# Performance work log

Hardware: AMD Instinct MI355X
Metric: run time of the kernel (lower is better)

The kernel has to match this reference:

```python
import jax, jax.numpy as jnp
import numpy as np

NUM_NODES = 100000
NUM_REL_P1 = 238  # num_relations + 1 (extra column for self-connection relation id -1)
B = 32768
S = 16
D_IN = 256
D_OUT = 256


def setup_inputs() -> dict:
    key = jax.random.key(0)
    k1, k2, k3, k4, k5 = jax.random.split(key, 5)
    neighbors = jax.random.randint(k1, (B, S), 0, NUM_NODES)          # sampled neighbor node ids
    relations = jax.random.randint(k2, (B, S), 0, NUM_REL_P1)          # sampled relation ids
    features = jax.random.normal(k3, (NUM_NODES, D_IN), dtype=jnp.float32)
    weight = jax.random.normal(k4, (D_OUT, D_IN), dtype=jnp.float32) * (1.0 / np.sqrt(D_IN))
    relation_weight = jax.random.normal(k5, (D_OUT, NUM_REL_P1), dtype=jnp.float32) * 0.05
    return {"neighbors": neighbors, "relations": relations, "features": features,
            "weight": weight, "relation_weight": relation_weight}


def reference(neighbors, relations, features, weight, relation_weight):
    # gather sampled neighbor embeddings: [B, S, D_in]
    neighbor_emb = features[neighbors]
    # mean-aggregate over the sample dim: [B, D_in]
    agg_neighbors = neighbor_emb.mean(axis=1)
    # linear transform: [B, D_in] @ [D_in, D_out] -> [B, D_out]
    agg_neighbors = agg_neighbors @ weight.T
    # gather + mean relation embeddings: [B, S, D_out] -> [B, D_out]
    agg_relations = relation_weight.T[relations].mean(axis=1)
    return jax.nn.relu(agg_neighbors + agg_relations)
```

## Files before the change

kernel.cpp:

```cpp
#include <hip/hip_runtime.h>

#define B_ROWS  32768
#define S_SAMP  16
#define NRELS   238
#define DIM     256
#define N_NODES 100000
#define NF4     ((N_NODES * DIM) / 4)
#define CONV_BLOCKS (NF4 / 256)

typedef __attribute__((ext_vector_type(8))) short  short8;
typedef __attribute__((ext_vector_type(8))) unsigned short ushort8;
typedef __attribute__((ext_vector_type(4))) float  f32x4;

static __device__ __forceinline__ unsigned short f2bf(float f) {
    unsigned int u = __float_as_uint(f);
    u += 0x7FFFu + ((u >> 16) & 1u);
    return (unsigned short)(u >> 16);
}
static __device__ __forceinline__ float bf2f(unsigned short u) {
    return __uint_as_float(((unsigned int)u) << 16);
}

__global__ __launch_bounds__(256) void prep_kernel(const float* __restrict__ F,
                                                   const float* __restrict__ W,
                                                   const float* __restrict__ RW,
                                                   unsigned short* __restrict__ Fb,
                                                   unsigned short* __restrict__ Wb,
                                                   unsigned short* __restrict__ RWb) {
    if (blockIdx.x < CONV_BLOCKS) {
        int i = blockIdx.x * 256 + threadIdx.x;
        float4 v = ((const float4*)F)[i];
        ushort4 p;
        p.x = f2bf(v.x); p.y = f2bf(v.y); p.z = f2bf(v.z); p.w = f2bf(v.w);
        ((ushort4*)Fb)[i] = p;
    } else {
        int i = (blockIdx.x - CONV_BLOCKS) * 256 + threadIdx.x;
        if (i < DIM * DIM) {
            Wb[i] = f2bf(W[i]);
            int n = i >> 8;
            int k = i & 255;
            RWb[i] = (k < NRELS) ? f2bf(RW[n * NRELS + k]) : (unsigned short)0;
        }
    }
}

__global__ __launch_bounds__(512, 8) void fused_kernel(const int* __restrict__ nbr,
                                                       const int* __restrict__ rels,
                                                       const unsigned short* __restrict__ Fb,
                                                       const unsigned short* __restrict__ RWb,
                                                       const unsigned short* __restrict__ Wb,
                                                       float* __restrict__ out) {
    __shared__ unsigned short As[32][264];
    __shared__ unsigned short Cs[32][264];
    __shared__ unsigned int   cnt4[32][32];
    const int tid  = threadIdx.x;
    const int lane = tid & 63;
    const int wid  = __builtin_amdgcn_readfirstlane(tid >> 6);
    const int half = lane >> 5;
    const int li   = lane & 31;
    const int col0 = lane & 15;
    const int quad = lane >> 4;
    const int r0g  = blockIdx.x * 32;

    unsigned int* c4 = (unsigned int*)cnt4;
    c4[tid] = 0u; c4[tid + 512] = 0u;
    __syncthreads();

    {
        int rid = rels[r0g * S_SAMP + tid];
        atomicAdd(&cnt4[tid >> 4][rid >> 3], 1u << ((rid & 7) * 4));
    }

    const float sc = 1.0f / 16.0f;
    for (int i = 0; i < 4; ++i) {
        const int row_l = wid * 4 + i;
        const int row_g = r0g + row_l;
        const int2* nb2 = (const int2*)(nbr + row_g * S_SAMP);
        float af[8] = {0.f, 0.f, 0.f, 0.f, 0.f, 0.f, 0.f, 0.f};
#pragma unroll
        for (int t = 0; t < 8; ++t) {
            int2 nn = nb2[t];
            int nid = half ? nn.y : nn.x;
            ushort8 f = *(const ushort8*)(Fb + (size_t)nid * DIM + li * 8);
#pragma unroll
            for (int j = 0; j < 8; ++j) af[j] += bf2f(f[j]);
        }
        ushort8 pk;
#pragma unroll
        for (int j = 0; j < 8; ++j) {
            float full = af[j] + __shfl_xor(af[j], 32, 64);
            pk[j] = f2bf(full * sc);
        }
        if (!half) *(ushort8*)&As[row_l][li * 8] = pk;
    }
    __syncthreads();

    {
        const int rr = tid >> 4;
        const int w2 = tid & 15;
#pragma unroll
        for (int g = 0; g < 2; ++g) {
            unsigned int w = cnt4[rr][w2 * 2 + g];
            ushort8 ck;
#pragma unroll
            for (int j = 0; j < 8; ++j)
                ck[j] = f2bf((float)((w >> (4 * j)) & 0xFu) * 0.0625f);
            *(ushort8*)&Cs[rr][(w2 * 2 + g) * 8] = ck;
        }
    }
    __syncthreads();

    f32x4 acc[2][2];
#pragma unroll
    for (int mt = 0; mt < 2; ++mt)
#pragma unroll
        for (int j = 0; j < 2; ++j) acc[mt][j] = (f32x4){0.f, 0.f, 0.f, 0.f};

#pragma unroll
    for (int s = 0; s < 2; ++s) {
        const unsigned short* Bp = s ? RWb : Wb;
#pragma unroll
        for (int kh = 0; kh < 4; ++kh) {
            short8 Breg[2][2];
#pragma unroll
            for (int j = 0; j < 2; ++j)
#pragma unroll
                for (int kk = 0; kk < 2; ++kk)
                    Breg[j][kk] = *(const short8*)(Bp + (size_t)((wid * 2 + j) * 16 + col0) * DIM
                                                      + (kh * 2 + kk) * 32 + quad * 8);
#pragma unroll
            for (int mt = 0; mt < 2; ++mt) {
                const int mrow = mt * 16 + col0;
#pragma unroll
                for (int kk = 0; kk < 2; ++kk) {
                    short8 a;
                    if (s == 0) a = *(const short8*)&As[mrow][(kh * 2 + kk) * 32 + quad * 8];
                    else        a = *(const short8*)&Cs[mrow][(kh * 2 + kk) * 32 + quad * 8];
#pragma unroll
                    for (int j = 0; j < 2; ++j)
                        acc[mt][j] = __builtin_amdgcn_mfma_f32_16x16x32_bf16(a, Breg[j][kk], acc[mt][j], 0, 0, 0);
                }
            }
        }
    }

#pragma unroll
    for (int mt = 0; mt < 2; ++mt) {
#pragma unroll
        for (int j = 0; j < 2; ++j) {
            const int col = (wid * 2 + j) * 16 + col0;
#pragma unroll
            for (int i2 = 0; i2 < 4; ++i2) {
                const int r_l = mt * 16 + quad * 4 + i2;
                float v = acc[mt][j][i2];
                out[(size_t)(r0g + r_l) * DIM + col] = v > 0.f ? v : 0.f;
            }
        }
    }
}

extern "C" void kernel_launch(void* const* d_in, const int* in_sizes, int n_in,
                              void* d_out, int out_size, void* d_ws, size_t ws_size,
                              hipStream_t stream) {
    const int*   neighbors = (const int*)d_in[0];
    const int*   relations = (const int*)d_in[1];
    const float* features  = (const float*)d_in[2];
    const float* weight    = (const float*)d_in[3];
    const float* relw      = (const float*)d_in[4];
    float* out = (float*)d_out;

    char* ws = (char*)d_ws;
    unsigned short* Wb  = (unsigned short*)ws;
    unsigned short* RWb = (unsigned short*)(ws + 131072);
    unsigned short* Fb  = (unsigned short*)(ws + 262144);

    prep_kernel<<<CONV_BLOCKS + 256, 256, 0, stream>>>(features, weight, relw, Fb, Wb, RWb);
    fused_kernel<<<B_ROWS / 32, 512, 0, stream>>>(neighbors, relations, Fb, RWb, Wb, out);
}
```

Before: 224.3 us.

## Shrink fused kernel tile to 16 rows with 256-thread blocks

```diff
diff --git a/kernel.cpp b/kernel.cpp
--- a/kernel.cpp
+++ b/kernel.cpp
@@ -44,15 +44,15 @@
     }
 }
 
-__global__ __launch_bounds__(512, 8) void fused_kernel(const int* __restrict__ nbr,
+__global__ __launch_bounds__(256, 8) void fused_kernel(const int* __restrict__ nbr,
                                                        const int* __restrict__ rels,
                                                        const unsigned short* __restrict__ Fb,
                                                        const unsigned short* __restrict__ RWb,
                                                        const unsigned short* __restrict__ Wb,
                                                        float* __restrict__ out) {
-    __shared__ unsigned short As[32][264];
-    __shared__ unsigned short Cs[32][264];
-    __shared__ unsigned int   cnt4[32][32];
+    __shared__ unsigned short As[16][264];
+    __shared__ unsigned short Cs[16][264];
+    __shared__ unsigned int   cnt4[16][32];
     const int tid  = threadIdx.x;
     const int lane = tid & 63;
     const int wid  = __builtin_amdgcn_readfirstlane(tid >> 6);
@@ -60,10 +60,10 @@
     const int li   = lane & 31;
     const int col0 = lane & 15;
     const int quad = lane >> 4;
-    const int r0g  = blockIdx.x * 32;
+    const int r0g  = blockIdx.x * 16;
 
     unsigned int* c4 = (unsigned int*)cnt4;
-    c4[tid] = 0u; c4[tid + 512] = 0u;
+    c4[tid] = 0u; c4[tid + 256] = 0u;
     __syncthreads();
 
     {
@@ -97,64 +97,48 @@
 
     {
         const int rr = tid >> 4;
-        const int w2 = tid & 15;
+        const int w2 = (tid & 15) * 2;
 #pragma unroll
         for (int g = 0; g < 2; ++g) {
-            unsigned int w = cnt4[rr][w2 * 2 + g];
+            unsigned int w = cnt4[rr][w2 + g];
             ushort8 ck;
 #pragma unroll
             for (int j = 0; j < 8; ++j)
                 ck[j] = f2bf((float)((w >> (4 * j)) & 0xFu) * 0.0625f);
-            *(ushort8*)&Cs[rr][(w2 * 2 + g) * 8] = ck;
+            *(ushort8*)&Cs[rr][(w2 + g) * 8] = ck;
         }
     }
     __syncthreads();
 
-    f32x4 acc[2][2];
+    f32x4 acc[4];
 #pragma unroll
-    for (int mt = 0; mt < 2; ++mt)
+    for (int j = 0; j < 4; ++j) acc[j] = (f32x4){0.f, 0.f, 0.f, 0.f};
+
+#pragma unroll 2
+    for (int ks = 0; ks < 16; ++ks) {
+        const unsigned short* Bp = (ks < 8) ? Wb : RWb;
+        const int kk = ks & 7;
+        short8 Breg[4];
 #pragma unroll
-        for (int j = 0; j < 2; ++j) acc[mt][j] = (f32x4){0.f, 0.f, 0.f, 0.f};
-
+        for (int j = 0; j < 4; ++j)
+            Breg[j] = *(const short8*)(Bp + (size_t)(wid * 64 + j * 16 + col0) * DIM
+                                          + kk * 32 + quad * 8);
+        short8 a;
+        if (ks < 8) a = *(const short8*)&As[col0][kk * 32 + quad * 8];
+        else        a = *(const short8*)&Cs[col0][kk * 32 + quad * 8];
 #pragma unroll
-    for (int s = 0; s < 2; ++s) {
-        const unsigned short* Bp = s ? RWb : Wb;
-#pragma unroll
-        for (int kh = 0; kh < 4; ++kh) {
-            short8 Breg[2][2];
-#pragma unroll
-            for (int j = 0; j < 2; ++j)
-#pragma unroll
-                for (int kk = 0; kk < 2; ++kk)
-                    Breg[j][kk] = *(const short8*)(Bp + (size_t)((wid * 2 + j) * 16 + col0) * DIM
-                                                      + (kh * 2 + kk) * 32 + quad * 8);
-#pragma unroll
-            for (int mt = 0; mt < 2; ++mt) {
-                const int mrow = mt * 16 + col0;
-#pragma unroll
-                for (int kk = 0; kk < 2; ++kk) {
-                    short8 a;
-                    if (s == 0) a = *(const short8*)&As[mrow][(kh * 2 + kk) * 32 + quad * 8];
-                    else        a = *(const short8*)&Cs[mrow][(kh * 2 + kk) * 32 + quad * 8];
-#pragma unroll
-                    for (int j = 0; j < 2; ++j)
-                        acc[mt][j] = __builtin_amdgcn_mfma_f32_16x16x32_bf16(a, Breg[j][kk], acc[mt][j], 0, 0, 0);
-                }
-            }
-        }
+        for (int j = 0; j < 4; ++j)
+            acc[j] = __builtin_amdgcn_mfma_f32_16x16x32_bf16(a, Breg[j], acc[j], 0, 0, 0);
     }
 
 #pragma unroll
-    for (int mt = 0; mt < 2; ++mt) {
+    for (int j = 0; j < 4; ++j) {
+        const int col = wid * 64 + j * 16 + col0;
 #pragma unroll
-        for (int j = 0; j < 2; ++j) {
-            const int col = (wid * 2 + j) * 16 + col0;
-#pragma unroll
-            for (int i2 = 0; i2 < 4; ++i2) {
-                const int r_l = mt * 16 + quad * 4 + i2;
-                float v = acc[mt][j][i2];
-                out[(size_t)(r0g + r_l) * DIM + col] = v > 0.f ? v : 0.f;
-            }
+        for (int i2 = 0; i2 < 4; ++i2) {
+            const int r_l = quad * 4 + i2;
+            float v = acc[j][i2];
+            out[(size_t)(r0g + r_l) * DIM + col] = v > 0.f ? v : 0.f;
         }
     }
 }
@@ -175,5 +159,5 @@
     unsigned short* Fb  = (unsigned short*)(ws + 262144);
 
     prep_kernel<<<CONV_BLOCKS + 256, 256, 0, stream>>>(features, weight, relw, Fb, Wb, RWb);
-    fused_kernel<<<B_ROWS / 32, 512, 0, stream>>>(neighbors, relations, Fb, RWb, Wb, out);
+    fused_kernel<<<B_ROWS / 16, 256, 0, stream>>>(neighbors, relations, Fb, RWb, Wb, out);
 }
```

Result: slower. 250.6 us (+11.7%).
